# Kernel optimization log

Hardware: AMD Instinct MI355X
Metric: run time of the kernel (lower is better)

Reference implementation:

```python
import jax, jax.numpy as jnp
import numpy as np

TEMPERATURE = 8.0  # sqrt(head_dim=64)


def sparsemax(z):
    """Sparsemax along the last axis (Martins & Astudillo 2016)."""
    S = z.shape[-1]
    z_sorted = -jnp.sort(-z, axis=-1)            # descending sort
    cs = jnp.cumsum(z_sorted, axis=-1)
    ks = jnp.arange(1, S + 1, dtype=z.dtype)
    support = 1.0 + ks * z_sorted > cs           # entries in the support set
    k_sup = jnp.sum(support, axis=-1, keepdims=True)  # support size >= 1
    tau = (jnp.take_along_axis(cs, k_sup - 1, axis=-1) - 1.0) / k_sup.astype(z.dtype)
    return jnp.maximum(z - tau, 0.0)


def setup_inputs() -> dict:
    key = jax.random.key(0)
    kq, kk, kv, km = jax.random.split(key, 4)
    B, Lq, Lk, D = 64, 1024, 1024, 64
    q = jax.random.normal(kq, (B, Lq, D), dtype=jnp.float32)
    k = jax.random.normal(kk, (B, Lk, D), dtype=jnp.float32)
    v = jax.random.normal(kv, (B, Lk, D), dtype=jnp.float32)
    mask = jax.random.randint(km, (B, Lq, Lk), 0, 2).astype(bool)  # True = masked out
    return {"q": q, "k": k, "v": v, "mask": mask}


def reference(q, k, v, mask):
    # scores: [B, Lq, Lk]
    attn = jnp.einsum('bqd,bkd->bqk', q / TEMPERATURE, k)
    # mask out disallowed keys with -inf
    attn = jnp.where(mask, -jnp.inf, attn)
    # rows where ALL keys are masked: set scores to 0 (avoids NaN in sparsemax)
    inf_mask = jnp.all(mask, axis=2, keepdims=True)  # [B, Lq, 1]
    attn = jnp.where(inf_mask, 0.0, attn)
    attn = sparsemax(attn)
    # zero out fully-masked rows again (dropout has p=0.0 -> identity in eval)
    attn = jnp.where(inf_mask, 0.0, attn)
    out = jnp.einsum('bqk,bkd->bqd', attn, v)
    return (out, attn)
```

## Files before the change

kernel.cpp:

```cpp
#include <hip/hip_runtime.h>
#include <float.h>


#define BATCH    64
#define SEQQ     1024
#define SEQK     1024
#define DHEAD    64

typedef short short8 __attribute__((ext_vector_type(8)));
typedef float f32x4  __attribute__((ext_vector_type(4)));
typedef unsigned short us4v __attribute__((ext_vector_type(4)));

typedef const __attribute__((address_space(1))) unsigned int as1_cuint;
typedef __attribute__((address_space(3))) unsigned int as3_uint;
typedef __attribute__((address_space(3))) unsigned char as3_uchar;

__device__ __forceinline__ unsigned short bf16_rne(float f) {
    unsigned u = __float_as_uint(f);
    u += 0x7fffu + ((u >> 16) & 1u);
    return (unsigned short)(u >> 16);
}

__device__ __forceinline__ void cvt_hilo8(const float* fv, float scale,
                                          short8* hi, short8* lo) {
    #pragma unroll
    for (int j = 0; j < 8; ++j) {
        float f = fv[j] * scale;
        unsigned short hb = bf16_rne(f);
        float hf = __uint_as_float((unsigned)hb << 16);
        (*hi)[j] = (short)hb;
        (*lo)[j] = (short)bf16_rne(f - hf);
    }
}

__global__ void detect_mask_fmt(const unsigned char* __restrict__ m,
                                int* __restrict__ flag) {
    __shared__ int s_found;
    if (threadIdx.x == 0) s_found = 0;
    __syncthreads();
    int found = 0;
    for (int o = threadIdx.x; o < 65536; o += 256) {
        if ((o & 3) != 0 && m[o] != 0) found = 1;
    }
    if (found) atomicOr(&s_found, 1);
    __syncthreads();
    if (threadIdx.x == 0) *flag = s_found;
}

__global__ __launch_bounds__(256) void kprep(
        const float* __restrict__ k, unsigned short* __restrict__ kbuf) {
    int gid  = blockIdx.x * 256 + threadIdx.x;
    int db   = gid & 7;
    int keyg = (gid >> 3) & 1023;
    int b    = gid >> 13;
    int kt   = keyg >> 7;
    int key  = keyg & 127;

    const float4* src =
        (const float4*)(k + ((size_t)b * SEQK + keyg) * DHEAD + db * 8);
    float4 f0 = src[0], f1 = src[1];
    float fv[8] = {f0.x, f0.y, f0.z, f0.w, f1.x, f1.y, f1.z, f1.w};
    short8 hi, lo;
    cvt_hilo8(fv, 1.0f, &hi, &lo);

    unsigned short* tile = kbuf + (size_t)(b * 8 + kt) * 16384;
    int off = key * 64 + ((db ^ (key & 7)) * 8);
    *(short8*)(tile + off)        = hi;
    *(short8*)(tile + 8192 + off) = lo;
}

__global__ __launch_bounds__(256) void score_kernel_dma(
        const float* __restrict__ q, const unsigned short* __restrict__ kbuf,
        unsigned short* __restrict__ sbuf, int pitch) {
    const int lane = threadIdx.x & 63;
    const int wave = threadIdx.x >> 6;
    const int quad = lane >> 4;
    const int l15  = lane & 15;
    const int qt = blockIdx.x >> 6;
    const int b  = blockIdx.x & 63;

    __shared__ unsigned short klds[2 * 128 * 64];

    const float* qrow =
        q + ((size_t)b * SEQQ + qt * 64 + wave * 16 + l15) * DHEAD;
    short8 a_hi[2], a_lo[2];
    #pragma unroll
    for (int kc = 0; kc < 2; ++kc) {
        const float4* src = (const float4*)(qrow + kc * 32 + quad * 8);
        float4 f0 = src[0], f1 = src[1];
        float fv[8] = {f0.x, f0.y, f0.z, f0.w, f1.x, f1.y, f1.z, f1.w};
        cvt_hilo8(fv, 0.125f, &a_hi[kc], &a_lo[kc]);
    }

    unsigned short* srow0 =
        sbuf + ((size_t)b * SEQQ + qt * 64 + wave * 16) * (size_t)pitch;

    for (int kt = 0; kt < 8; ++kt) {
        __syncthreads();
        const unsigned char* gtile =
            (const unsigned char*)(kbuf + (size_t)(b * 8 + kt) * 16384);
        {
            unsigned base = wave * 8192 + lane * 16;
            #pragma unroll
            for (int j = 0; j < 8; ++j) {
                unsigned off = base + j * 1024;
                as1_cuint* gp = (as1_cuint*)(gtile + off);
                as3_uint*  lp = (as3_uint*)((as3_uchar*)klds +
                                            (wave * 8192 + j * 1024));
                __builtin_amdgcn_global_load_lds(gp, lp, 16, 0, 0);
            }
        }
        __syncthreads();

        unsigned short* srow = srow0 + kt * 128;
        #pragma unroll
        for (int g = 0; g < 8; ++g) {
            int key = g * 16 + l15;
            short8 b_hi[2], b_lo[2];
            #pragma unroll
            for (int kc = 0; kc < 2; ++kc) {
                int db  = kc * 4 + quad;
                int off = key * 64 + ((db ^ (key & 7)) * 8);
                b_hi[kc] = *(const short8*)(klds + off);
                b_lo[kc] = *(const short8*)(klds + 8192 + off);
            }
            f32x4 acc = {0.f, 0.f, 0.f, 0.f};
            #pragma unroll
            for (int kc = 0; kc < 2; ++kc) {
                acc = __builtin_amdgcn_mfma_f32_16x16x32_bf16(a_hi[kc], b_hi[kc], acc, 0, 0, 0);
                acc = __builtin_amdgcn_mfma_f32_16x16x32_bf16(a_lo[kc], b_hi[kc], acc, 0, 0, 0);
                acc = __builtin_amdgcn_mfma_f32_16x16x32_bf16(a_hi[kc], b_lo[kc], acc, 0, 0, 0);
            }
            #pragma unroll
            for (int r = 0; r < 4; ++r)
                srow[(size_t)(quad * 4 + r) * (size_t)pitch + g * 16 + l15] =
                    bf16_rne(acc[r]);
        }
    }
}

__global__ __launch_bounds__(256) void score_kernel_cvt(
        const float* __restrict__ q, const float* __restrict__ k,
        unsigned short* __restrict__ sbuf, int pitch) {
    const int lane = threadIdx.x & 63;
    const int wave = threadIdx.x >> 6;
    const int quad = lane >> 4;
    const int l15  = lane & 15;
    const int qt = blockIdx.x >> 6;
    const int b  = blockIdx.x & 63;

    __shared__ unsigned short klds[2 * 128 * 64];

    const float* qrow =
        q + ((size_t)b * SEQQ + qt * 64 + wave * 16 + l15) * DHEAD;
    short8 a_hi[2], a_lo[2];
    #pragma unroll
    for (int kc = 0; kc < 2; ++kc) {
        const float4* src = (const float4*)(qrow + kc * 32 + quad * 8);
        float4 f0 = src[0], f1 = src[1];
        float fv[8] = {f0.x, f0.y, f0.z, f0.w, f1.x, f1.y, f1.z, f1.w};
        cvt_hilo8(fv, 0.125f, &a_hi[kc], &a_lo[kc]);
    }

    const float* kb = k + (size_t)b * SEQK * DHEAD;
    unsigned short* srow0 =
        sbuf + ((size_t)b * SEQQ + qt * 64 + wave * 16) * (size_t)pitch;

    for (int kt = 0; kt < 8; ++kt) {
        __syncthreads();
        const float* kbase = kb + (size_t)kt * 128 * DHEAD;
        #pragma unroll
        for (int it = 0; it < 4; ++it) {
            int e   = threadIdx.x + 256 * it;
            int key = e >> 3, db = e & 7;
            const float4* src = (const float4*)(kbase + key * DHEAD + db * 8);
            float4 f0 = src[0], f1 = src[1];
            float fv[8] = {f0.x, f0.y, f0.z, f0.w, f1.x, f1.y, f1.z, f1.w};
            short8 hi, lo;
            cvt_hilo8(fv, 1.0f, &hi, &lo);
            int off = key * 64 + ((db ^ (key & 7)) * 8);
            *(short8*)(klds + off)        = hi;
            *(short8*)(klds + 8192 + off) = lo;
        }
        __syncthreads();

        unsigned short* srow = srow0 + kt * 128;
        #pragma unroll
        for (int g = 0; g < 8; ++g) {
            int key = g * 16 + l15;
            short8 b_hi[2], b_lo[2];
            #pragma unroll
            for (int kc = 0; kc < 2; ++kc) {
                int db  = kc * 4 + quad;
                int off = key * 64 + ((db ^ (key & 7)) * 8);
                b_hi[kc] = *(const short8*)(klds + off);
                b_lo[kc] = *(const short8*)(klds + 8192 + off);
            }
            f32x4 acc = {0.f, 0.f, 0.f, 0.f};
            #pragma unroll
            for (int kc = 0; kc < 2; ++kc) {
                acc = __builtin_amdgcn_mfma_f32_16x16x32_bf16(a_hi[kc], b_hi[kc], acc, 0, 0, 0);
                acc = __builtin_amdgcn_mfma_f32_16x16x32_bf16(a_lo[kc], b_hi[kc], acc, 0, 0, 0);
                acc = __builtin_amdgcn_mfma_f32_16x16x32_bf16(a_hi[kc], b_lo[kc], acc, 0, 0, 0);
            }
            #pragma unroll
            for (int r = 0; r < 4; ++r)
                srow[(size_t)(quad * 4 + r) * (size_t)pitch + g * 16 + l15] =
                    bf16_rne(acc[r]);
        }
    }
}

__global__ __launch_bounds__(256) void sparsemax_pv(
        const float* __restrict__ v, const void* __restrict__ mask,
        const int* __restrict__ fmt_flag,
        float* __restrict__ out, float* __restrict__ attn,
        const unsigned short* __restrict__ sbuf, int pitch) {
    const int lane = threadIdx.x & 63;
    const int wave = threadIdx.x >> 6;
    const int row  = blockIdx.x * 4 + wave;
    const int b    = row >> 10;
    float* arow = attn + (size_t)row * SEQK;
    const int mask_is_byte = fmt_flag ? *fmt_flag : 1;

    __shared__ float pbuf[4][SEQK];

    const us4v* s4 = (const us4v*)(sbuf + (size_t)row * (size_t)pitch);
    float s[16];
    #pragma unroll
    for (int t = 0; t < 4; ++t) {
        us4v u = __builtin_nontemporal_load(s4 + lane + 64 * t);
        s[4*t+0] = __uint_as_float((unsigned)u[0] << 16);
        s[4*t+1] = __uint_as_float((unsigned)u[1] << 16);
        s[4*t+2] = __uint_as_float((unsigned)u[2] << 16);
        s[4*t+3] = __uint_as_float((unsigned)u[3] << 16);
    }
    if (mask_is_byte) {
        const unsigned* m32 =
            (const unsigned*)((const unsigned char*)mask + (size_t)row * SEQK);
        #pragma unroll
        for (int t = 0; t < 4; ++t) {
            unsigned m = __builtin_nontemporal_load(m32 + lane + 64 * t);
            if (m & 0x000000ffu) s[4*t+0] = -FLT_MAX;
            if (m & 0x0000ff00u) s[4*t+1] = -FLT_MAX;
            if (m & 0x00ff0000u) s[4*t+2] = -FLT_MAX;
            if (m & 0xff000000u) s[4*t+3] = -FLT_MAX;
        }
    } else {
        const int* mi = (const int*)mask + (size_t)row * SEQK;
        #pragma unroll
        for (int t = 0; t < 4; ++t) {
            int m0 = __builtin_nontemporal_load(mi + 4 * (lane + 64 * t) + 0);
            int m1 = __builtin_nontemporal_load(mi + 4 * (lane + 64 * t) + 1);
            int m2 = __builtin_nontemporal_load(mi + 4 * (lane + 64 * t) + 2);
            int m3 = __builtin_nontemporal_load(mi + 4 * (lane + 64 * t) + 3);
            if (m0) s[4*t+0] = -FLT_MAX;
            if (m1) s[4*t+1] = -FLT_MAX;
            if (m2) s[4*t+2] = -FLT_MAX;
            if (m3) s[4*t+3] = -FLT_MAX;
        }
    }

    float mx = -FLT_MAX;
    #pragma unroll
    for (int i = 0; i < 16; ++i) mx = fmaxf(mx, s[i]);
    #pragma unroll
    for (int off = 32; off >= 1; off >>= 1)
        mx = fmaxf(mx, __shfl_xor(mx, off, 64));

    if (mx <= -FLT_MAX) {
        f32x4 z = {0.f, 0.f, 0.f, 0.f};
        #pragma unroll
        for (int t = 0; t < 4; ++t)
            __builtin_nontemporal_store(z, (f32x4*)arow + lane + 64 * t);
        out[(size_t)row * DHEAD + lane] = 0.f;
        return;
    }

    float thr = mx - 1.0f, tau = 0.f;
    int cnt_prev = -1;
    for (int it = 0; it < 32; ++it) {
        float lsum = 0.f; int lcnt = 0;
        #pragma unroll
        for (int i = 0; i < 16; ++i)
            if (s[i] > thr) { lsum += s[i]; lcnt++; }
        #pragma unroll
        for (int off = 32; off >= 1; off >>= 1) {
            lsum += __shfl_xor(lsum, off, 64);
            lcnt += __shfl_xor(lcnt, off, 64);
        }
        tau = (lsum - 1.0f) / (float)lcnt;
        if (lcnt == cnt_prev) break;
        cnt_prev = lcnt;
        thr = tau;
    }

    float p[16];
    #pragma unroll
    for (int i = 0; i < 16; ++i) {
        float pv = s[i] - tau;
        p[i] = pv > 0.f ? pv : 0.f;
    }
    #pragma unroll
    for (int t = 0; t < 4; ++t) {
        f32x4 f = {p[4*t+0], p[4*t+1], p[4*t+2], p[4*t+3]};
        __builtin_nontemporal_store(f, (f32x4*)arow + lane + 64 * t);
        *(f32x4*)&pbuf[wave][4 * (lane + 64 * t)] = f;
    }

    const float* vbase = v + (size_t)b * SEQK * DHEAD;
    float oacc = 0.f;
    #pragma unroll
    for (int t = 0; t < 4; ++t) {
        #pragma unroll
        for (int c = 0; c < 4; ++c) {
            int i = 4 * t + c;
            unsigned long long mb = __ballot(p[i] > 0.f);
            while (mb) {
                int k0, k1 = -1, k2 = -1, k3 = -1;
                k0 = __ffsll(mb) - 1; mb &= mb - 1;
                if (mb) { k1 = __ffsll(mb) - 1; mb &= mb - 1; }
                if (mb) { k2 = __ffsll(mb) - 1; mb &= mb - 1; }
                if (mb) { k3 = __ffsll(mb) - 1; mb &= mb - 1; }
                int key0 = 4 * k0 + 256 * t + c;
                float pj0 = pbuf[wave][key0];
                float v0  = vbase[(size_t)key0 * DHEAD + lane];
                float pj1 = 0.f, pj2 = 0.f, pj3 = 0.f;
                float v1 = 0.f, v2 = 0.f, v3 = 0.f;
                if (k1 >= 0) {
                    int key1 = 4 * k1 + 256 * t + c;
                    pj1 = pbuf[wave][key1];
                    v1  = vbase[(size_t)key1 * DHEAD + lane];
                }
                if (k2 >= 0) {
                    int key2 = 4 * k2 + 256 * t + c;
                    pj2 = pbuf[wave][key2];
                    v2  = vbase[(size_t)key2 * DHEAD + lane];
                }
                if (k3 >= 0) {
                    int key3 = 4 * k3 + 256 * t + c;
                    pj3 = pbuf[wave][key3];
                    v3  = vbase[(size_t)key3 * DHEAD + lane];
                }
                oacc = fmaf(pj0, v0, oacc);
                if (k1 >= 0) oacc = fmaf(pj1, v1, oacc);
                if (k2 >= 0) oacc = fmaf(pj2, v2, oacc);
                if (k3 >= 0) oacc = fmaf(pj3, v3, oacc);
            }
        }
    }
    out[(size_t)row * DHEAD + lane] = oacc;
}

extern "C" void kernel_launch(void* const* d_in, const int* in_sizes, int n_in,
                              void* d_out, int out_size, void* d_ws, size_t ws_size,
                              hipStream_t stream) {
    const float* q = (const float*)d_in[0];
    const float* k = (const float*)d_in[1];
    const float* v = (const float*)d_in[2];
    const void*  m = d_in[3];

    float* out  = (float*)d_out;
    float* attn = out + (size_t)BATCH * SEQQ * DHEAD;

    int* flag = nullptr;
    if (ws_size >= sizeof(int)) {
        flag = (int*)d_ws;
        detect_mask_fmt<<<1, 256, 0, stream>>>((const unsigned char*)m, flag);
    }

    const size_t S_BYTES = (size_t)BATCH * SEQQ * SEQK * 2;
    const size_t K_BYTES = (size_t)BATCH * SEQK * DHEAD * 2 * 2;

    unsigned short* sbuf;
    int pitch;
    bool s_in_ws = ws_size >= 16 + S_BYTES;
    if (s_in_ws) {
        sbuf  = (unsigned short*)d_ws + 8;
        pitch = SEQK;
    } else {
        sbuf  = (unsigned short*)attn;
        pitch = 2 * SEQK;
    }

    bool k_in_ws = s_in_ws && ws_size >= 16 + S_BYTES + K_BYTES;
    if (k_in_ws) {
        unsigned short* kbuf =
            (unsigned short*)((char*)d_ws + 16 + S_BYTES);
        kprep<<<(BATCH * SEQK * 8) / 256, 256, 0, stream>>>(k, kbuf);
        score_kernel_dma<<<(SEQQ / 64) * BATCH, 256, 0, stream>>>(
            q, kbuf, sbuf, pitch);
    } else {
        score_kernel_cvt<<<(SEQQ / 64) * BATCH, 256, 0, stream>>>(
            q, k, sbuf, pitch);
    }

    sparsemax_pv<<<(BATCH * SEQQ) / 4, 256, 0, stream>>>(
        v, m, flag, out, attn, sbuf, pitch);
}
```

Baseline: 643.0 us.

## Fuse score GEMM with sparsemax and PV into one kernel via LDS

Merges the score kernel and the sparsemax/PV kernel into a single fused kernel. Each block computes a 32-row by 1024-key bf16 score tile into LDS (64 KB), then runs sparsemax and sparse PV from that tile, so the global score buffer round-trip goes away. K tiles shrink to 64 keys, and the per-wave probability buffer is replaced by lane shuffles. The trade-offs are heavy LDS use limiting occupancy, and serial per-row sparsemax work per wave after the GEMM phase.

```diff
diff --git a/kernel.cpp b/kernel.cpp
--- a/kernel.cpp
+++ b/kernel.cpp
@@ -53,8 +53,8 @@
     int db   = gid & 7;
     int keyg = (gid >> 3) & 1023;
     int b    = gid >> 13;
-    int kt   = keyg >> 7;
-    int key  = keyg & 127;
+    int kt   = keyg >> 6;
+    int key  = keyg & 63;
 
     const float4* src =
         (const float4*)(k + ((size_t)b * SEQK + keyg) * DHEAD + db * 8);
@@ -63,15 +63,19 @@
     short8 hi, lo;
     cvt_hilo8(fv, 1.0f, &hi, &lo);
 
-    unsigned short* tile = kbuf + (size_t)(b * 8 + kt) * 16384;
+    unsigned short* tile = kbuf + (size_t)(b * 16 + kt) * 8192;
     int off = key * 64 + ((db ^ (key & 7)) * 8);
     *(short8*)(tile + off)        = hi;
-    *(short8*)(tile + 8192 + off) = lo;
-}
-
-__global__ __launch_bounds__(256) void score_kernel_dma(
-        const float* __restrict__ q, const unsigned short* __restrict__ kbuf,
-        unsigned short* __restrict__ sbuf, int pitch) {
+    *(short8*)(tile + 4096 + off) = lo;
+}
+
+template<bool DMA>
+__global__ __launch_bounds__(256, 2) void fused_attn(
+        const float* __restrict__ q, const float* __restrict__ kmat,
+        const unsigned short* __restrict__ kbuf,
+        const float* __restrict__ v, const void* __restrict__ mask,
+        const int* __restrict__ fmt_flag,
+        float* __restrict__ out, float* __restrict__ attn) {
     const int lane = threadIdx.x & 63;
     const int wave = threadIdx.x >> 6;
     const int quad = lane >> 4;
@@ -79,10 +83,14 @@
     const int qt = blockIdx.x >> 6;
     const int b  = blockIdx.x & 63;
 
-    __shared__ unsigned short klds[2 * 128 * 64];
+    __shared__ unsigned short slds[32 * 1024];
+    __shared__ unsigned short klds[8192];
+
+    const int rowg = wave & 1;
+    const int keyh = wave >> 1;
 
     const float* qrow =
-        q + ((size_t)b * SEQQ + qt * 64 + wave * 16 + l15) * DHEAD;
+        q + ((size_t)b * SEQQ + qt * 32 + rowg * 16 + l15) * DHEAD;
     short8 a_hi[2], a_lo[2];
     #pragma unroll
     for (int kc = 0; kc < 2; ++kc) {
@@ -92,29 +100,42 @@
         cvt_hilo8(fv, 0.125f, &a_hi[kc], &a_lo[kc]);
     }
 
-    unsigned short* srow0 =
-        sbuf + ((size_t)b * SEQQ + qt * 64 + wave * 16) * (size_t)pitch;
-
-    for (int kt = 0; kt < 8; ++kt) {
+    for (int kt = 0; kt < 16; ++kt) {
         __syncthreads();
-        const unsigned char* gtile =
-            (const unsigned char*)(kbuf + (size_t)(b * 8 + kt) * 16384);
-        {
-            unsigned base = wave * 8192 + lane * 16;
-            #pragma unroll
-            for (int j = 0; j < 8; ++j) {
-                unsigned off = base + j * 1024;
-                as1_cuint* gp = (as1_cuint*)(gtile + off);
-                as3_uint*  lp = (as3_uint*)((as3_uchar*)klds +
-                                            (wave * 8192 + j * 1024));
+        if (DMA) {
+            const unsigned char* gtile =
+                (const unsigned char*)(kbuf + (size_t)(b * 16 + kt) * 8192);
+            #pragma unroll
+            for (int j = 0; j < 4; ++j) {
+                unsigned off = wave * 4096 + j * 1024;
+                as1_cuint* gp = (as1_cuint*)(gtile + off + lane * 16);
+                as3_uint*  lp = (as3_uint*)((as3_uchar*)klds + off);
                 __builtin_amdgcn_global_load_lds(gp, lp, 16, 0, 0);
             }
+        } else {
+            const float* kbase =
+                kmat + ((size_t)b * SEQK + kt * 64) * DHEAD;
+            #pragma unroll
+            for (int it = 0; it < 2; ++it) {
+                int e   = threadIdx.x + 256 * it;
+                int key = e >> 3, db = e & 7;
+                const float4* src =
+                    (const float4*)(kbase + key * DHEAD + db * 8);
+                float4 f0 = src[0], f1 = src[1];
+                float fv[8] = {f0.x, f0.y, f0.z, f0.w,
+                               f1.x, f1.y, f1.z, f1.w};
+                short8 hi, lo;
+                cvt_hilo8(fv, 1.0f, &hi, &lo);
+                int off = key * 64 + ((db ^ (key & 7)) * 8);
+                *(short8*)(klds + off)        = hi;
+                *(short8*)(klds + 4096 + off) = lo;
+            }
         }
         __syncthreads();
 
-        unsigned short* srow = srow0 + kt * 128;
-        #pragma unroll
-        for (int g = 0; g < 8; ++g) {
+        #pragma unroll
+        for (int gg = 0; gg < 2; ++gg) {
+            int g   = keyh * 2 + gg;
             int key = g * 16 + l15;
             short8 b_hi[2], b_lo[2];
             #pragma unroll
@@ -122,7 +143,7 @@
                 int db  = kc * 4 + quad;
                 int off = key * 64 + ((db ^ (key & 7)) * 8);
                 b_hi[kc] = *(const short8*)(klds + off);
-                b_lo[kc] = *(const short8*)(klds + 8192 + off);
+                b_lo[kc] = *(const short8*)(klds + 4096 + off);
             }
             f32x4 acc = {0.f, 0.f, 0.f, 0.f};
             #pragma unroll
@@ -133,223 +154,150 @@
             }
             #pragma unroll
             for (int r = 0; r < 4; ++r)
-                srow[(size_t)(quad * 4 + r) * (size_t)pitch + g * 16 + l15] =
-                    bf16_rne(acc[r]);
-        }
-    }
-}
-
-__global__ __launch_bounds__(256) void score_kernel_cvt(
-        const float* __restrict__ q, const float* __restrict__ k,
-        unsigned short* __restrict__ sbuf, int pitch) {
-    const int lane = threadIdx.x & 63;
-    const int wave = threadIdx.x >> 6;
-    const int quad = lane >> 4;
-    const int l15  = lane & 15;
-    const int qt = blockIdx.x >> 6;
-    const int b  = blockIdx.x & 63;
-
-    __shared__ unsigned short klds[2 * 128 * 64];
-
-    const float* qrow =
-        q + ((size_t)b * SEQQ + qt * 64 + wave * 16 + l15) * DHEAD;
-    short8 a_hi[2], a_lo[2];
-    #pragma unroll
-    for (int kc = 0; kc < 2; ++kc) {
-        const float4* src = (const float4*)(qrow + kc * 32 + quad * 8);
-        float4 f0 = src[0], f1 = src[1];
-        float fv[8] = {f0.x, f0.y, f0.z, f0.w, f1.x, f1.y, f1.z, f1.w};
-        cvt_hilo8(fv, 0.125f, &a_hi[kc], &a_lo[kc]);
-    }
-
-    const float* kb = k + (size_t)b * SEQK * DHEAD;
-    unsigned short* srow0 =
-        sbuf + ((size_t)b * SEQQ + qt * 64 + wave * 16) * (size_t)pitch;
-
-    for (int kt = 0; kt < 8; ++kt) {
-        __syncthreads();
-        const float* kbase = kb + (size_t)kt * 128 * DHEAD;
-        #pragma unroll
-        for (int it = 0; it < 4; ++it) {
-            int e   = threadIdx.x + 256 * it;
-            int key = e >> 3, db = e & 7;
-            const float4* src = (const float4*)(kbase + key * DHEAD + db * 8);
-            float4 f0 = src[0], f1 = src[1];
-            float fv[8] = {f0.x, f0.y, f0.z, f0.w, f1.x, f1.y, f1.z, f1.w};
-            short8 hi, lo;
-            cvt_hilo8(fv, 1.0f, &hi, &lo);
-            int off = key * 64 + ((db ^ (key & 7)) * 8);
-            *(short8*)(klds + off)        = hi;
-            *(short8*)(klds + 8192 + off) = lo;
-        }
-        __syncthreads();
-
-        unsigned short* srow = srow0 + kt * 128;
-        #pragma unroll
-        for (int g = 0; g < 8; ++g) {
-            int key = g * 16 + l15;
-            short8 b_hi[2], b_lo[2];
-            #pragma unroll
-            for (int kc = 0; kc < 2; ++kc) {
-                int db  = kc * 4 + quad;
-                int off = key * 64 + ((db ^ (key & 7)) * 8);
-                b_hi[kc] = *(const short8*)(klds + off);
-                b_lo[kc] = *(const short8*)(klds + 8192 + off);
-            }
-            f32x4 acc = {0.f, 0.f, 0.f, 0.f};
-            #pragma unroll
-            for (int kc = 0; kc < 2; ++kc) {
-                acc = __builtin_amdgcn_mfma_f32_16x16x32_bf16(a_hi[kc], b_hi[kc], acc, 0, 0, 0);
-                acc = __builtin_amdgcn_mfma_f32_16x16x32_bf16(a_lo[kc], b_hi[kc], acc, 0, 0, 0);
-                acc = __builtin_amdgcn_mfma_f32_16x16x32_bf16(a_hi[kc], b_lo[kc], acc, 0, 0, 0);
-            }
-            #pragma unroll
-            for (int r = 0; r < 4; ++r)
-                srow[(size_t)(quad * 4 + r) * (size_t)pitch + g * 16 + l15] =
-                    bf16_rne(acc[r]);
-        }
-    }
-}
-
-__global__ __launch_bounds__(256) void sparsemax_pv(
-        const float* __restrict__ v, const void* __restrict__ mask,
-        const int* __restrict__ fmt_flag,
-        float* __restrict__ out, float* __restrict__ attn,
-        const unsigned short* __restrict__ sbuf, int pitch) {
-    const int lane = threadIdx.x & 63;
-    const int wave = threadIdx.x >> 6;
-    const int row  = blockIdx.x * 4 + wave;
-    const int b    = row >> 10;
-    float* arow = attn + (size_t)row * SEQK;
+                slds[(rowg * 16 + quad * 4 + r) * 1024 +
+                     kt * 64 + g * 16 + l15] = bf16_rne(acc[r]);
+        }
+    }
+    __syncthreads();
+
     const int mask_is_byte = fmt_flag ? *fmt_flag : 1;
-
-    __shared__ float pbuf[4][SEQK];
-
-    const us4v* s4 = (const us4v*)(sbuf + (size_t)row * (size_t)pitch);
-    float s[16];
-    #pragma unroll
-    for (int t = 0; t < 4; ++t) {
-        us4v u = __builtin_nontemporal_load(s4 + lane + 64 * t);
-        s[4*t+0] = __uint_as_float((unsigned)u[0] << 16);
-        s[4*t+1] = __uint_as_float((unsigned)u[1] << 16);
-        s[4*t+2] = __uint_as_float((unsigned)u[2] << 16);
-        s[4*t+3] = __uint_as_float((unsigned)u[3] << 16);
-    }
-    if (mask_is_byte) {
-        const unsigned* m32 =
-            (const unsigned*)((const unsigned char*)mask + (size_t)row * SEQK);
+    const float* vbase = v + (size_t)b * SEQK * DHEAD;
+
+    for (int rr = 0; rr < 8; ++rr) {
+        const int    lrow = wave * 8 + rr;
+        const size_t grow = (size_t)b * SEQQ + qt * 32 + lrow;
+        float* arow = attn + grow * SEQK;
+
+        unsigned mby[4];
+        int mi32[16];
+        if (mask_is_byte) {
+            const unsigned* m32 =
+                (const unsigned*)((const unsigned char*)mask + grow * SEQK);
+            #pragma unroll
+            for (int t = 0; t < 4; ++t)
+                mby[t] = __builtin_nontemporal_load(m32 + lane + 64 * t);
+        } else {
+            const int* mi = (const int*)mask + grow * SEQK;
+            #pragma unroll
+            for (int t = 0; t < 4; ++t) {
+                #pragma unroll
+                for (int c = 0; c < 4; ++c)
+                    mi32[4*t+c] = __builtin_nontemporal_load(
+                        mi + 4 * (lane + 64 * t) + c);
+            }
+        }
+
+        float s[16];
+        {
+            const us4v* s4 = (const us4v*)(slds + lrow * 1024);
+            #pragma unroll
+            for (int t = 0; t < 4; ++t) {
+                us4v u = s4[lane + 64 * t];
+                s[4*t+0] = __uint_as_float((unsigned)u[0] << 16);
+                s[4*t+1] = __uint_as_float((unsigned)u[1] << 16);
+                s[4*t+2] = __uint_as_float((unsigned)u[2] << 16);
+                s[4*t+3] = __uint_as_float((unsigned)u[3] << 16);
+            }
+        }
+
+        if (mask_is_byte) {
+            #pragma unroll
+            for (int t = 0; t < 4; ++t) {
+                if (mby[t] & 0x000000ffu) s[4*t+0] = -FLT_MAX;
+                if (mby[t] & 0x0000ff00u) s[4*t+1] = -FLT_MAX;
+                if (mby[t] & 0x00ff0000u) s[4*t+2] = -FLT_MAX;
+                if (mby[t] & 0xff000000u) s[4*t+3] = -FLT_MAX;
+            }
+        } else {
+            #pragma unroll
+            for (int i = 0; i < 16; ++i)
+                if (mi32[i]) s[i] = -FLT_MAX;
+        }
+
+        float mx = -FLT_MAX;
+        #pragma unroll
+        for (int i = 0; i < 16; ++i) mx = fmaxf(mx, s[i]);
+        #pragma unroll
+        for (int off = 32; off >= 1; off >>= 1)
+            mx = fmaxf(mx, __shfl_xor(mx, off, 64));
+
+        if (mx <= -FLT_MAX) {
+            f32x4 z = {0.f, 0.f, 0.f, 0.f};
+            #pragma unroll
+            for (int t = 0; t < 4; ++t)
+                __builtin_nontemporal_store(z, (f32x4*)arow + lane + 64 * t);
+            out[grow * DHEAD + lane] = 0.f;
+            continue;
+        }
+
+        float thr = mx - 1.0f, tau = 0.f;
+        int cnt_prev = -1;
+        for (int it = 0; it < 32; ++it) {
+            float lsum = 0.f; int lcnt = 0;
+            #pragma unroll
+            for (int i = 0; i < 16; ++i)
+                if (s[i] > thr) { lsum += s[i]; lcnt++; }
+            #pragma unroll
+            for (int off = 32; off >= 1; off >>= 1) {
+                lsum += __shfl_xor(lsum, off, 64);
+                lcnt += __shfl_xor(lcnt, off, 64);
+            }
+            tau = (lsum - 1.0f) / (float)lcnt;
+            if (lcnt == cnt_prev) break;
+            cnt_prev = lcnt;
+            thr = tau;
+        }
+
+        float p[16];
+        #pragma unroll
+        for (int i = 0; i < 16; ++i) {
+            float pv = s[i] - tau;
+            p[i] = pv > 0.f ? pv : 0.f;
+        }
         #pragma unroll
         for (int t = 0; t < 4; ++t) {
-            unsigned m = __builtin_nontemporal_load(m32 + lane + 64 * t);
-            if (m & 0x000000ffu) s[4*t+0] = -FLT_MAX;
-            if (m & 0x0000ff00u) s[4*t+1] = -FLT_MAX;
-            if (m & 0x00ff0000u) s[4*t+2] = -FLT_MAX;
-            if (m & 0xff000000u) s[4*t+3] = -FLT_MAX;
-        }
-    } else {
-        const int* mi = (const int*)mask + (size_t)row * SEQK;
+            f32x4 f = {p[4*t+0], p[4*t+1], p[4*t+2], p[4*t+3]};
+            __builtin_nontemporal_store(f, (f32x4*)arow + lane + 64 * t);
+        }
+
+        float oacc = 0.f;
         #pragma unroll
         for (int t = 0; t < 4; ++t) {
-            int m0 = __builtin_nontemporal_load(mi + 4 * (lane + 64 * t) + 0);
-            int m1 = __builtin_nontemporal_load(mi + 4 * (lane + 64 * t) + 1);
-            int m2 = __builtin_nontemporal_load(mi + 4 * (lane + 64 * t) + 2);
-            int m3 = __builtin_nontemporal_load(mi + 4 * (lane + 64 * t) + 3);
-            if (m0) s[4*t+0] = -FLT_MAX;
-            if (m1) s[4*t+1] = -FLT_MAX;
-            if (m2) s[4*t+2] = -FLT_MAX;
-            if (m3) s[4*t+3] = -FLT_MAX;
-        }
-    }
-
-    float mx = -FLT_MAX;
-    #pragma unroll
-    for (int i = 0; i < 16; ++i) mx = fmaxf(mx, s[i]);
-    #pragma unroll
-    for (int off = 32; off >= 1; off >>= 1)
-        mx = fmaxf(mx, __shfl_xor(mx, off, 64));
-
-    if (mx <= -FLT_MAX) {
-        f32x4 z = {0.f, 0.f, 0.f, 0.f};
-        #pragma unroll
-        for (int t = 0; t < 4; ++t)
-            __builtin_nontemporal_store(z, (f32x4*)arow + lane + 64 * t);
-        out[(size_t)row * DHEAD + lane] = 0.f;
-        return;
-    }
-
-    float thr = mx - 1.0f, tau = 0.f;
-    int cnt_prev = -1;
-    for (int it = 0; it < 32; ++it) {
-        float lsum = 0.f; int lcnt = 0;
-        #pragma unroll
-        for (int i = 0; i < 16; ++i)
-            if (s[i] > thr) { lsum += s[i]; lcnt++; }
-        #pragma unroll
-        for (int off = 32; off >= 1; off >>= 1) {
-            lsum += __shfl_xor(lsum, off, 64);
-            lcnt += __shfl_xor(lcnt, off, 64);
-        }
-        tau = (lsum - 1.0f) / (float)lcnt;
-        if (lcnt == cnt_prev) break;
-        cnt_prev = lcnt;
-        thr = tau;
-    }
-
-    float p[16];
-    #pragma unroll
-    for (int i = 0; i < 16; ++i) {
-        float pv = s[i] - tau;
-        p[i] = pv > 0.f ? pv : 0.f;
-    }
-    #pragma unroll
-    for (int t = 0; t < 4; ++t) {
-        f32x4 f = {p[4*t+0], p[4*t+1], p[4*t+2], p[4*t+3]};
-        __builtin_nontemporal_store(f, (f32x4*)arow + lane + 64 * t);
-        *(f32x4*)&pbuf[wave][4 * (lane + 64 * t)] = f;
-    }
-
-    const float* vbase = v + (size_t)b * SEQK * DHEAD;
-    float oacc = 0.f;
-    #pragma unroll
-    for (int t = 0; t < 4; ++t) {
-        #pragma unroll
-        for (int c = 0; c < 4; ++c) {
-            int i = 4 * t + c;
-            unsigned long long mb = __ballot(p[i] > 0.f);
-            while (mb) {
-                int k0, k1 = -1, k2 = -1, k3 = -1;
-                k0 = __ffsll(mb) - 1; mb &= mb - 1;
-                if (mb) { k1 = __ffsll(mb) - 1; mb &= mb - 1; }
-                if (mb) { k2 = __ffsll(mb) - 1; mb &= mb - 1; }
-                if (mb) { k3 = __ffsll(mb) - 1; mb &= mb - 1; }
-                int key0 = 4 * k0 + 256 * t + c;
-                float pj0 = pbuf[wave][key0];
-                float v0  = vbase[(size_t)key0 * DHEAD + lane];
-                float pj1 = 0.f, pj2 = 0.f, pj3 = 0.f;
-                float v1 = 0.f, v2 = 0.f, v3 = 0.f;
-                if (k1 >= 0) {
-                    int key1 = 4 * k1 + 256 * t + c;
-                    pj1 = pbuf[wave][key1];
-                    v1  = vbase[(size_t)key1 * DHEAD + lane];
+            #pragma unroll
+            for (int c = 0; c < 4; ++c) {
+                int i = 4 * t + c;
+                unsigned long long mb = __ballot(p[i] > 0.f);
+                while (mb) {
+                    int k0, k1 = -1, k2 = -1, k3 = -1;
+                    k0 = __ffsll(mb) - 1; mb &= mb - 1;
+                    if (mb) { k1 = __ffsll(mb) - 1; mb &= mb - 1; }
+                    if (mb) { k2 = __ffsll(mb) - 1; mb &= mb - 1; }
+                    if (mb) { k3 = __ffsll(mb) - 1; mb &= mb - 1; }
+                    float pj0 = __shfl(p[i], k0);
+                    float v0  = vbase[(size_t)(4 * k0 + 256 * t + c) * DHEAD + lane];
+                    float pj1 = 0.f, pj2 = 0.f, pj3 = 0.f;
+                    float v1 = 0.f, v2 = 0.f, v3 = 0.f;
+                    if (k1 >= 0) {
+                        pj1 = __shfl(p[i], k1);
+                        v1  = vbase[(size_t)(4 * k1 + 256 * t + c) * DHEAD + lane];
+                    }
+                    if (k2 >= 0) {
+                        pj2 = __shfl(p[i], k2);
+                        v2  = vbase[(size_t)(4 * k2 + 256 * t + c) * DHEAD + lane];
+                    }
+                    if (k3 >= 0) {
+                        pj3 = __shfl(p[i], k3);
+                        v3  = vbase[(size_t)(4 * k3 + 256 * t + c) * DHEAD + lane];
+                    }
+                    oacc = fmaf(pj0, v0, oacc);
+                    if (k1 >= 0) oacc = fmaf(pj1, v1, oacc);
+                    if (k2 >= 0) oacc = fmaf(pj2, v2, oacc);
+                    if (k3 >= 0) oacc = fmaf(pj3, v3, oacc);
                 }
-                if (k2 >= 0) {
-                    int key2 = 4 * k2 + 256 * t + c;
-                    pj2 = pbuf[wave][key2];
-                    v2  = vbase[(size_t)key2 * DHEAD + lane];
-                }
-                if (k3 >= 0) {
-                    int key3 = 4 * k3 + 256 * t + c;
-                    pj3 = pbuf[wave][key3];
-                    v3  = vbase[(size_t)key3 * DHEAD + lane];
-                }
-                oacc = fmaf(pj0, v0, oacc);
-                if (k1 >= 0) oacc = fmaf(pj1, v1, oacc);
-                if (k2 >= 0) oacc = fmaf(pj2, v2, oacc);
-                if (k3 >= 0) oacc = fmaf(pj3, v3, oacc);
-            }
-        }
-    }
-    out[(size_t)row * DHEAD + lane] = oacc;
+            }
+        }
+        out[grow * DHEAD + lane] = oacc;
+    }
 }
 
 extern "C" void kernel_launch(void* const* d_in, const int* in_sizes, int n_in,
@@ -369,32 +317,15 @@
         detect_mask_fmt<<<1, 256, 0, stream>>>((const unsigned char*)m, flag);
     }
 
-    const size_t S_BYTES = (size_t)BATCH * SEQQ * SEQK * 2;
     const size_t K_BYTES = (size_t)BATCH * SEQK * DHEAD * 2 * 2;
 
-    unsigned short* sbuf;
-    int pitch;
-    bool s_in_ws = ws_size >= 16 + S_BYTES;
-    if (s_in_ws) {
-        sbuf  = (unsigned short*)d_ws + 8;
-        pitch = SEQK;
+    if (ws_size >= 16 + K_BYTES) {
+        unsigned short* kbuf = (unsigned short*)((char*)d_ws + 16);
+        kprep<<<(BATCH * SEQK * 8) / 256, 256, 0, stream>>>(k, kbuf);
+        fused_attn<true><<<(SEQQ / 32) * BATCH, 256, 0, stream>>>(
+            q, k, kbuf, v, m, flag, out, attn);
     } else {
-        sbuf  = (unsigned short*)attn;
-        pitch = 2 * SEQK;
-    }
-
-    bool k_in_ws = s_in_ws && ws_size >= 16 + S_BYTES + K_BYTES;
-    if (k_in_ws) {
-        unsigned short* kbuf =
-            (unsigned short*)((char*)d_ws + 16 + S_BYTES);
-        kprep<<<(BATCH * SEQK * 8) / 256, 256, 0, stream>>>(k, kbuf);
-        score_kernel_dma<<<(SEQQ / 64) * BATCH, 256, 0, stream>>>(
-            q, kbuf, sbuf, pitch);
-    } else {
-        score_kernel_cvt<<<(SEQQ / 64) * BATCH, 256, 0, stream>>>(
-            q, k, sbuf, pitch);
-    }
-
-    sparsemax_pv<<<(BATCH * SEQQ) / 4, 256, 0, stream>>>(
-        v, m, flag, out, attn, sbuf, pitch);
-}
+        fused_attn<false><<<(SEQQ / 32) * BATCH, 256, 0, stream>>>(
+            q, k, nullptr, v, m, flag, out, attn);
+    }
+}
```

After: 722.3 us. +12.3%, slower.

## Transpose MFMA operands for row-contiguous score stores, fuse mask detect, drop LDS pbuf

Applied to the files above, without the earlier changes.

The score kernels swap the MFMA A/B operands so each lane holds four consecutive keys of one query row. That lets them write packed 8-byte bf16 vectors instead of scattered 2-byte stores strided by pitch. The mask-format detection kernel is folded into an extra block of the K-prep kernel, saving one launch. The sparsemax PV kernel drops its shared-memory probability buffer and fetches weights through wave shuffles, which reduces LDS traffic and shared memory use.

```diff
diff --git a/kernel.cpp b/kernel.cpp
--- a/kernel.cpp
+++ b/kernel.cpp
@@ -47,8 +47,23 @@
     if (threadIdx.x == 0) *flag = s_found;
 }
 
-__global__ __launch_bounds__(256) void kprep(
-        const float* __restrict__ k, unsigned short* __restrict__ kbuf) {
+__global__ __launch_bounds__(256) void kprep_detect(
+        const float* __restrict__ k, unsigned short* __restrict__ kbuf,
+        const unsigned char* __restrict__ m, int* __restrict__ flag) {
+    if (blockIdx.x == (BATCH * SEQK * 8) / 256) {
+        __shared__ int s_found;
+        if (threadIdx.x == 0) s_found = 0;
+        __syncthreads();
+        int found = 0;
+        for (int o = threadIdx.x; o < 65536; o += 256) {
+            if ((o & 3) != 0 && m[o] != 0) found = 1;
+        }
+        if (found) atomicOr(&s_found, 1);
+        __syncthreads();
+        if (threadIdx.x == 0) *flag = s_found;
+        return;
+    }
+
     int gid  = blockIdx.x * 256 + threadIdx.x;
     int db   = gid & 7;
     int keyg = (gid >> 3) & 1023;
@@ -92,8 +107,8 @@
         cvt_hilo8(fv, 0.125f, &a_hi[kc], &a_lo[kc]);
     }
 
-    unsigned short* srow0 =
-        sbuf + ((size_t)b * SEQQ + qt * 64 + wave * 16) * (size_t)pitch;
+    unsigned short* srowq =
+        sbuf + ((size_t)b * SEQQ + qt * 64 + wave * 16 + l15) * (size_t)pitch;
 
     for (int kt = 0; kt < 8; ++kt) {
         __syncthreads();
@@ -112,7 +127,6 @@
         }
         __syncthreads();
 
-        unsigned short* srow = srow0 + kt * 128;
         #pragma unroll
         for (int g = 0; g < 8; ++g) {
             int key = g * 16 + l15;
@@ -127,14 +141,14 @@
             f32x4 acc = {0.f, 0.f, 0.f, 0.f};
             #pragma unroll
             for (int kc = 0; kc < 2; ++kc) {
-                acc = __builtin_amdgcn_mfma_f32_16x16x32_bf16(a_hi[kc], b_hi[kc], acc, 0, 0, 0);
-                acc = __builtin_amdgcn_mfma_f32_16x16x32_bf16(a_lo[kc], b_hi[kc], acc, 0, 0, 0);
-                acc = __builtin_amdgcn_mfma_f32_16x16x32_bf16(a_hi[kc], b_lo[kc], acc, 0, 0, 0);
-            }
-            #pragma unroll
-            for (int r = 0; r < 4; ++r)
-                srow[(size_t)(quad * 4 + r) * (size_t)pitch + g * 16 + l15] =
-                    bf16_rne(acc[r]);
+                acc = __builtin_amdgcn_mfma_f32_16x16x32_bf16(b_hi[kc], a_hi[kc], acc, 0, 0, 0);
+                acc = __builtin_amdgcn_mfma_f32_16x16x32_bf16(b_hi[kc], a_lo[kc], acc, 0, 0, 0);
+                acc = __builtin_amdgcn_mfma_f32_16x16x32_bf16(b_lo[kc], a_hi[kc], acc, 0, 0, 0);
+            }
+            us4v pk;
+            #pragma unroll
+            for (int r = 0; r < 4; ++r) pk[r] = bf16_rne(acc[r]);
+            *(us4v*)(srowq + kt * 128 + g * 16 + quad * 4) = pk;
         }
     }
 }
@@ -163,8 +177,8 @@
     }
 
     const float* kb = k + (size_t)b * SEQK * DHEAD;
-    unsigned short* srow0 =
-        sbuf + ((size_t)b * SEQQ + qt * 64 + wave * 16) * (size_t)pitch;
+    unsigned short* srowq =
+        sbuf + ((size_t)b * SEQQ + qt * 64 + wave * 16 + l15) * (size_t)pitch;
 
     for (int kt = 0; kt < 8; ++kt) {
         __syncthreads();
@@ -184,7 +198,6 @@
         }
         __syncthreads();
 
-        unsigned short* srow = srow0 + kt * 128;
         #pragma unroll
         for (int g = 0; g < 8; ++g) {
             int key = g * 16 + l15;
@@ -199,14 +212,14 @@
             f32x4 acc = {0.f, 0.f, 0.f, 0.f};
             #pragma unroll
             for (int kc = 0; kc < 2; ++kc) {
-                acc = __builtin_amdgcn_mfma_f32_16x16x32_bf16(a_hi[kc], b_hi[kc], acc, 0, 0, 0);
-                acc = __builtin_amdgcn_mfma_f32_16x16x32_bf16(a_lo[kc], b_hi[kc], acc, 0, 0, 0);
-                acc = __builtin_amdgcn_mfma_f32_16x16x32_bf16(a_hi[kc], b_lo[kc], acc, 0, 0, 0);
-            }
-            #pragma unroll
-            for (int r = 0; r < 4; ++r)
-                srow[(size_t)(quad * 4 + r) * (size_t)pitch + g * 16 + l15] =
-                    bf16_rne(acc[r]);
+                acc = __builtin_amdgcn_mfma_f32_16x16x32_bf16(b_hi[kc], a_hi[kc], acc, 0, 0, 0);
+                acc = __builtin_amdgcn_mfma_f32_16x16x32_bf16(b_hi[kc], a_lo[kc], acc, 0, 0, 0);
+                acc = __builtin_amdgcn_mfma_f32_16x16x32_bf16(b_lo[kc], a_hi[kc], acc, 0, 0, 0);
+            }
+            us4v pk;
+            #pragma unroll
+            for (int r = 0; r < 4; ++r) pk[r] = bf16_rne(acc[r]);
+            *(us4v*)(srowq + kt * 128 + g * 16 + quad * 4) = pk;
         }
     }
 }
@@ -223,8 +236,6 @@
     float* arow = attn + (size_t)row * SEQK;
     const int mask_is_byte = fmt_flag ? *fmt_flag : 1;
 
-    __shared__ float pbuf[4][SEQK];
-
     const us4v* s4 = (const us4v*)(sbuf + (size_t)row * (size_t)pitch);
     float s[16];
     #pragma unroll
@@ -305,7 +316,6 @@
     for (int t = 0; t < 4; ++t) {
         f32x4 f = {p[4*t+0], p[4*t+1], p[4*t+2], p[4*t+3]};
         __builtin_nontemporal_store(f, (f32x4*)arow + lane + 64 * t);
-        *(f32x4*)&pbuf[wave][4 * (lane + 64 * t)] = f;
     }
 
     const float* vbase = v + (size_t)b * SEQK * DHEAD;
@@ -322,25 +332,21 @@
                 if (mb) { k1 = __ffsll(mb) - 1; mb &= mb - 1; }
                 if (mb) { k2 = __ffsll(mb) - 1; mb &= mb - 1; }
                 if (mb) { k3 = __ffsll(mb) - 1; mb &= mb - 1; }
-                int key0 = 4 * k0 + 256 * t + c;
-                float pj0 = pbuf[wave][key0];
-                float v0  = vbase[(size_t)key0 * DHEAD + lane];
+                float pj0 = __shfl(p[i], k0);
+                float v0  = vbase[(size_t)(4 * k0 + 256 * t + c) * DHEAD + lane];
                 float pj1 = 0.f, pj2 = 0.f, pj3 = 0.f;
                 float v1 = 0.f, v2 = 0.f, v3 = 0.f;
                 if (k1 >= 0) {
-                    int key1 = 4 * k1 + 256 * t + c;
-                    pj1 = pbuf[wave][key1];
-                    v1  = vbase[(size_t)key1 * DHEAD + lane];
+                    pj1 = __shfl(p[i], k1);
+                    v1  = vbase[(size_t)(4 * k1 + 256 * t + c) * DHEAD + lane];
                 }
                 if (k2 >= 0) {
-                    int key2 = 4 * k2 + 256 * t + c;
-                    pj2 = pbuf[wave][key2];
-                    v2  = vbase[(size_t)key2 * DHEAD + lane];
+                    pj2 = __shfl(p[i], k2);
+                    v2  = vbase[(size_t)(4 * k2 + 256 * t + c) * DHEAD + lane];
                 }
                 if (k3 >= 0) {
-                    int key3 = 4 * k3 + 256 * t + c;
-                    pj3 = pbuf[wave][key3];
-                    v3  = vbase[(size_t)key3 * DHEAD + lane];
+                    pj3 = __shfl(p[i], k3);
+                    v3  = vbase[(size_t)(4 * k3 + 256 * t + c) * DHEAD + lane];
                 }
                 oacc = fmaf(pj0, v0, oacc);
                 if (k1 >= 0) oacc = fmaf(pj1, v1, oacc);
@@ -364,10 +370,7 @@
     float* attn = out + (size_t)BATCH * SEQQ * DHEAD;
 
     int* flag = nullptr;
-    if (ws_size >= sizeof(int)) {
-        flag = (int*)d_ws;
-        detect_mask_fmt<<<1, 256, 0, stream>>>((const unsigned char*)m, flag);
-    }
+    if (ws_size >= sizeof(int)) flag = (int*)d_ws;
 
     const size_t S_BYTES = (size_t)BATCH * SEQQ * SEQK * 2;
     const size_t K_BYTES = (size_t)BATCH * SEQK * DHEAD * 2 * 2;
@@ -387,10 +390,13 @@
     if (k_in_ws) {
         unsigned short* kbuf =
             (unsigned short*)((char*)d_ws + 16 + S_BYTES);
-        kprep<<<(BATCH * SEQK * 8) / 256, 256, 0, stream>>>(k, kbuf);
+        kprep_detect<<<(BATCH * SEQK * 8) / 256 + 1, 256, 0, stream>>>(
+            k, kbuf, (const unsigned char*)m, flag);
         score_kernel_dma<<<(SEQQ / 64) * BATCH, 256, 0, stream>>>(
             q, kbuf, sbuf, pitch);
     } else {
+        if (flag)
+            detect_mask_fmt<<<1, 256, 0, stream>>>((const unsigned char*)m, flag);
         score_kernel_cvt<<<(SEQQ / 64) * BATCH, 256, 0, stream>>>(
             q, k, sbuf, pitch);
     }
```

Measured after the change: 641.6 us (median of 2 runs). About the same (-0.2%).
